# Performance work log

Hardware: AMD Instinct MI355X
Metric: run time of the kernel (lower is better)

The kernel has to match this reference:

```python
import jax, jax.numpy as jnp
import numpy as np

# module hyperparameters (from init_kwargs)
STRIDE, PAD, DIL = 1, 1, 1
GROUPS, DG = 1, 1
KH, KW = 3, 3
CIN, COUT = 256, 256


def _mdcn_forward(x, offset, mask, weight, bias):
    B, C, H, W = x.shape
    Cout = weight.shape[0]
    K = KH * KW
    Ho = (H + 2 * PAD - (DIL * (KH - 1) + 1)) // STRIDE + 1
    Wo = (W + 2 * PAD - (DIL * (KW - 1) + 1)) // STRIDE + 1
    Cg = C // DG

    # offset channel layout: ((g*K + k)*2 + {0: dy, 1: dx})
    off = offset.reshape(B, DG, KH, KW, 2, Ho, Wo)
    base_y = (jnp.arange(Ho) * STRIDE - PAD)[None, :] + DIL * jnp.arange(KH)[:, None]  # [KH,Ho]
    base_x = (jnp.arange(Wo) * STRIDE - PAD)[None, :] + DIL * jnp.arange(KW)[:, None]  # [KW,Wo]
    sy = base_y[None, None, :, None, :, None].astype(x.dtype) + off[:, :, :, :, 0]  # [B,DG,KH,KW,Ho,Wo]
    sx = base_x[None, None, None, :, None, :].astype(x.dtype) + off[:, :, :, :, 1]

    y0f = jnp.floor(sy); x0f = jnp.floor(sx)
    wy = sy - y0f; wx = sx - x0f
    y0 = y0f.astype(jnp.int32); x0 = x0f.astype(jnp.int32)

    xg = x.reshape(B, DG, Cg, H * W)

    def corner(yc, xc, w):
        valid = (yc >= 0) & (yc < H) & (xc >= 0) & (xc < W)
        idx = jnp.clip(yc, 0, H - 1) * W + jnp.clip(xc, 0, W - 1)  # [B,DG,KH,KW,Ho,Wo]
        v = jnp.take_along_axis(xg, idx.reshape(B, DG, 1, -1), axis=3)  # [B,DG,Cg,K*Ho*Wo]
        v = v.reshape(B, DG, Cg, KH, KW, Ho, Wo)
        return v * (w * valid.astype(x.dtype))[:, :, None]

    val = (corner(y0, x0, (1 - wy) * (1 - wx))
           + corner(y0, x0 + 1, (1 - wy) * wx)
           + corner(y0 + 1, x0, wy * (1 - wx))
           + corner(y0 + 1, x0 + 1, wy * wx))  # [B,DG,Cg,KH,KW,Ho,Wo]

    cols = val * mask.reshape(B, DG, 1, KH, KW, Ho, Wo)
    cols = cols.reshape(B, GROUPS, (C // GROUPS) * K, Ho * Wo)
    wg = weight.reshape(GROUPS, Cout // GROUPS, (C // GROUPS) * K)
    out = jnp.einsum('gok,bgkp->bgop', wg, cols).reshape(B, Cout, Ho, Wo)
    return out + bias[None, :, None, None]


def setup_inputs() -> dict:
    key = jax.random.key(0)
    k1, k2, k3, k4 = jax.random.split(key, 4)
    B, H, W = 4, 64, 64
    x = jax.random.normal(k1, (B, CIN, H, W), dtype=jnp.float32)
    offset = jax.random.normal(k2, (B, 2 * DG * KH * KW, H, W), dtype=jnp.float32)
    mask = jax.random.uniform(k3, (B, DG * KH * KW, H, W), dtype=jnp.float32)
    stdv = 1.0 / np.sqrt(CIN * KH * KW)
    weight = jax.random.uniform(k4, (COUT, CIN // GROUPS, KH, KW), dtype=jnp.float32,
                                minval=-stdv, maxval=stdv)
    bias = jnp.zeros((COUT,), dtype=jnp.float32)
    return {"x": x, "offset": offset, "mask": mask, "weight": weight, "bias": bias}


def reference(x, offset, mask, weight, bias):
    return _mdcn_forward(x, offset, mask, weight, bias)
```

## Files before the change

### kernel.cpp

```cpp
#include <hip/hip_runtime.h>
#include <hip/hip_bf16.h>
#include <stdint.h>

#define KDIM 2304

typedef __bf16 bf16_t;
typedef bf16_t bf16x8 __attribute__((ext_vector_type(8)));
typedef float f32x4 __attribute__((ext_vector_type(4)));
typedef float f32x2 __attribute__((ext_vector_type(2)));

__device__ __forceinline__ float b2f_lo(uint32_t u) {
  union { uint32_t i; float f; } c; c.i = u << 16; return c.f;
}
__device__ __forceinline__ float b2f_hi(uint32_t u) {
  union { uint32_t i; float f; } c; c.i = u & 0xffff0000u; return c.f;
}
__device__ __forceinline__ uint32_t pk_bf16(float a, float b) {
  __hip_bfloat162 h = __float22bfloat162_rn(make_float2(a, b));
  union { __hip_bfloat162 h; uint32_t u; } c; c.h = h; return c.u;
}

__global__ __launch_bounds__(256) void k_prep(const float* __restrict__ x,
                                              uint16_t* __restrict__ xt,
                                              const float* __restrict__ w,
                                              uint16_t* __restrict__ wt2) {
  int tid = threadIdx.x;
  if (blockIdx.x < 2048) {
    __shared__ float tile[32][65];
    int b = blockIdx.x >> 9;
    int cgrp = (blockIdx.x >> 6) & 7;
    int sgrp = blockIdx.x & 63;
    int c0 = cgrp << 5, s0 = sgrp << 6;
#pragma unroll
    for (int it = 0; it < 2; ++it) {
      int f = tid + it * 256;
      int rr = f >> 4, col = (f & 15) << 2;
      float4 v = *(const float4*)&x[((size_t)(b * 256 + c0 + rr)) * 4096 + s0 + col];
      tile[rr][col + 0] = v.x;
      tile[rr][col + 1] = v.y;
      tile[rr][col + 2] = v.z;
      tile[rr][col + 3] = v.w;
    }
    __syncthreads();
    int sp = tid >> 2, cg = tid & 3;
    uint4 o;
    o.x = pk_bf16(tile[cg * 8 + 0][sp], tile[cg * 8 + 1][sp]);
    o.y = pk_bf16(tile[cg * 8 + 2][sp], tile[cg * 8 + 3][sp]);
    o.z = pk_bf16(tile[cg * 8 + 4][sp], tile[cg * 8 + 5][sp]);
    o.w = pk_bf16(tile[cg * 8 + 6][sp], tile[cg * 8 + 7][sp]);
    *(uint4*)&xt[((size_t)b * 4096 + s0 + sp) * 256 + c0 + cg * 8] = o;
  } else {
    int i = blockIdx.x - 2048;
    int tap = i >> 2, w64 = i & 3;
    uint16_t* dst = wt2 + (size_t)i * 16384;
#pragma unroll
    for (int s = 0; s < 8; ++s) {
      int slot = tid + s * 256;
      int lane = slot & 63;
      int kh = (slot >> 6) & 1, strip = slot >> 7;
      int row = strip * 16 + (lane & 15);
      int cin0 = w64 * 64 + kh * 32 + ((lane >> 4) << 3);
      const float* src = w + (size_t)row * KDIM + (size_t)cin0 * 9 + tap;
      uint4 o;
      o.x = pk_bf16(src[0 * 9], src[1 * 9]);
      o.y = pk_bf16(src[2 * 9], src[3 * 9]);
      o.z = pk_bf16(src[4 * 9], src[5 * 9]);
      o.w = pk_bf16(src[6 * 9], src[7 * 9]);
      *(uint4*)(dst + (size_t)slot * 8) = o;
    }
  }
}

__device__ __forceinline__ void mk_corners(int tap, int p, int ho,
                                           const float* s_off, const float* s_msk,
                                           float cw[4], int cpo[4]) {
  int kh = tap / 3, kw = tap - kh * 3;
  float dy = s_off[(2 * tap) * 64 + p];
  float dx = s_off[(2 * tap + 1) * 64 + p];
  float mm = s_msk[tap * 64 + p];
  float sy = (float)(ho - 1 + kh) + dy;
  float sx = (float)(p - 1 + kw) + dx;
  float fy = floorf(sy), fx = floorf(sx);
  int y0 = (int)fy, x0 = (int)fx;
  float wy = sy - fy, wx = sx - fx;
#pragma unroll
  for (int cy = 0; cy < 2; ++cy) {
#pragma unroll
    for (int cx = 0; cx < 2; ++cx) {
      int y = y0 + cy, xx = x0 + cx;
      float wgt = (cy ? wy : 1.f - wy) * (cx ? wx : 1.f - wx) * mm;
      bool v = ((unsigned)y < 64u) && ((unsigned)xx < 64u);
      wgt = v ? wgt : 0.f;
      int yc = min(max(y, 0), 63), xc = min(max(xx, 0), 63);
      cw[cy * 2 + cx] = wgt;
      cpo[cy * 2 + cx] = ((yc << 6) + xc) * 256;
    }
  }
}

__global__ __launch_bounds__(1024, 4) void k_fused(const uint16_t* __restrict__ xt,
                                                   const uint16_t* __restrict__ wt2,
                                                   const float* __restrict__ off,
                                                   const float* __restrict__ msk,
                                                   const float* __restrict__ bias,
                                                   float* __restrict__ out) {
  __shared__ __align__(16) uint16_t Bs[2][64][64];
  __shared__ float s_off[18 * 64];
  __shared__ float s_msk[9 * 64];

  int tid = threadIdx.x;
  int swz = ((int)blockIdx.x & 7) * 32 + ((int)blockIdx.x >> 3);
  int b = swz >> 6, ho = swz & 63;

  const float* offb = off + (size_t)b * 18 * 4096 + ho * 64;
  for (int i = tid; i < 18 * 64; i += 1024)
    s_off[i] = offb[(size_t)(i >> 6) * 4096 + (i & 63)];
  const float* mskb = msk + (size_t)b * 9 * 4096 + ho * 64;
  for (int i = tid; i < 9 * 64; i += 1024)
    s_msk[i] = mskb[(size_t)(i >> 6) * 4096 + (i & 63)];

  int lane = tid & 63, strip = tid >> 6;
  int q = lane >> 4, r = lane & 15;
  int p = tid >> 4, cg = tid & 15;
  const uint16_t* xtb = xt + (size_t)b * 4096 * 256 + cg * 4;
  int bcol = (((cg >> 1) ^ (p & 7)) << 3) + ((cg & 1) << 2);

  f32x4 acc[4];
#pragma unroll
  for (int ni = 0; ni < 4; ++ni) acc[ni] = f32x4{0.f, 0.f, 0.f, 0.f};

  __syncthreads();

  float cw[4];
  int cpo[4];
  uint2 dnv[4];
  bf16x8 AFA[2], AFB[2];

  int c0 = (q ^ (r & 7)) << 3;
  int c1 = c0 ^ 32;

  mk_corners(0, p, ho, s_off, s_msk, cw, cpo);
#pragma unroll
  for (int c = 0; c < 4; ++c) dnv[c] = *(const uint2*)(xtb + cpo[c]);
  {
    const uint16_t* wp = wt2 + strip * 1024 + lane * 8;
    AFA[0] = *(const bf16x8*)(wp);
    AFA[1] = *(const bf16x8*)(wp + 512);
  }
  {
    f32x2 a0 = {0.f, 0.f}, a1 = {0.f, 0.f};
#pragma unroll
    for (int c = 0; c < 4; ++c) {
      f32x2 wc = {cw[c], cw[c]};
      a0 += wc * f32x2{b2f_lo(dnv[c].x), b2f_hi(dnv[c].x)};
      a1 += wc * f32x2{b2f_lo(dnv[c].y), b2f_hi(dnv[c].y)};
    }
    uint2 o;
    o.x = pk_bf16(a0.x, a0.y);
    o.y = pk_bf16(a1.x, a1.y);
    *(uint2*)&Bs[0][p][bcol] = o;
  }
  __syncthreads();

#define BODY(IEXPR, AFC, AFN)                                                   \
  {                                                                             \
    const int i_ = (IEXPR);                                                     \
    if (i_ < 35) {                                                              \
      int nx = i_ + 1;                                                          \
      if ((nx & 3) == 0) mk_corners(nx >> 2, p, ho, s_off, s_msk, cw, cpo);     \
      int chw = (nx & 3) << 6;                                                  \
      _Pragma("unroll")                                                         \
      for (int c = 0; c < 4; ++c) dnv[c] = *(const uint2*)(xtb + cpo[c] + chw); \
      const uint16_t* wp = wt2 + (size_t)nx * 16384 + strip * 1024 + lane * 8;  \
      AFN[0] = *(const bf16x8*)(wp);                                            \
      AFN[1] = *(const bf16x8*)(wp + 512);                                      \
    }                                                                           \
    {                                                                           \
      const uint16_t* bsrow = &Bs[(IEXPR) & 1][0][0];                           \
      _Pragma("unroll")                                                         \
      for (int ni = 0; ni < 4; ++ni) {                                          \
        bf16x8 b0 = *(const bf16x8*)(bsrow + (ni * 16 + r) * 64 + c0);          \
        bf16x8 b1 = *(const bf16x8*)(bsrow + (ni * 16 + r) * 64 + c1);          \
        acc[ni] = __builtin_amdgcn_mfma_f32_16x16x32_bf16(AFC[0], b0, acc[ni], 0, 0, 0); \
        acc[ni] = __builtin_amdgcn_mfma_f32_16x16x32_bf16(AFC[1], b1, acc[ni], 0, 0, 0); \
      }                                                                         \
    }                                                                           \
    if (i_ < 35) {                                                              \
      f32x2 a0 = {0.f, 0.f}, a1 = {0.f, 0.f};                                   \
      _Pragma("unroll")                                                         \
      for (int c = 0; c < 4; ++c) {                                             \
        f32x2 wc = {cw[c], cw[c]};                                              \
        a0 += wc * f32x2{b2f_lo(dnv[c].x), b2f_hi(dnv[c].x)};                   \
        a1 += wc * f32x2{b2f_lo(dnv[c].y), b2f_hi(dnv[c].y)};                   \
      }                                                                         \
      uint2 o;                                                                  \
      o.x = pk_bf16(a0.x, a0.y);                                                \
      o.y = pk_bf16(a1.x, a1.y);                                                \
      *(uint2*)&Bs[1 - ((IEXPR) & 1)][p][bcol] = o;                             \
    }                                                                           \
    __syncthreads();                                                            \
  }

#pragma unroll 1
  for (int ii = 0; ii < 18; ++ii) {
    BODY(2 * ii, AFA, AFB);
    BODY(2 * ii + 1, AFB, AFA);
  }
#undef BODY

#pragma unroll
  for (int j = 0; j < 4; ++j) {
    int m = strip * 16 + q * 4 + j;
    float bv = bias[m];
#pragma unroll
    for (int ni = 0; ni < 4; ++ni) {
      out[((size_t)(b * 256 + m)) * 4096 + ho * 64 + ni * 16 + r] = acc[ni][j] + bv;
    }
  }
}

extern "C" void kernel_launch(void* const* d_in, const int* in_sizes, int n_in,
                              void* d_out, int out_size, void* d_ws, size_t ws_size,
                              hipStream_t stream) {
  (void)in_sizes; (void)n_in; (void)out_size; (void)ws_size;
  const float* x      = (const float*)d_in[0];
  const float* offset = (const float*)d_in[1];
  const float* mask   = (const float*)d_in[2];
  const float* weight = (const float*)d_in[3];
  const float* bias   = (const float*)d_in[4];
  float* out = (float*)d_out;

  uint8_t* ws = (uint8_t*)d_ws;
  uint16_t* xt  = (uint16_t*)ws;
  uint16_t* wt2 = (uint16_t*)(ws + 8388608);

  k_prep<<<dim3(2084), 256, 0, stream>>>(x, xt, weight, wt2);
  k_fused<<<dim3(256), 1024, 0, stream>>>(xt, wt2, offset, mask, bias, out);
}
```

Measured before the change: 133.4 us.

## Deepen gather prefetch to two stages and coalesce weight repack via LDS

The fused kernel's main loop now prefetches the bilinear corner gathers two iterations ahead, using double-buffered corner weights and offsets, and is unrolled over tap groups with statically resolved buffers. It also issues all B-fragment LDS reads before the MFMAs and raises wave priority around them. The weight-prep blocks now use one block per output row, staging the row in shared memory so global reads are coalesced instead of strided. This costs more registers, which may reduce occupancy, and makes the loop schedule more complex.

```diff
diff --git a/kernel.cpp b/kernel.cpp
--- a/kernel.cpp
+++ b/kernel.cpp
@@ -50,23 +50,25 @@
     o.w = pk_bf16(tile[cg * 8 + 6][sp], tile[cg * 8 + 7][sp]);
     *(uint4*)&xt[((size_t)b * 4096 + s0 + sp) * 256 + c0 + cg * 8] = o;
   } else {
-    int i = blockIdx.x - 2048;
-    int tap = i >> 2, w64 = i & 3;
-    uint16_t* dst = wt2 + (size_t)i * 16384;
-#pragma unroll
-    for (int s = 0; s < 8; ++s) {
-      int slot = tid + s * 256;
-      int lane = slot & 63;
-      int kh = (slot >> 6) & 1, strip = slot >> 7;
-      int row = strip * 16 + (lane & 15);
-      int cin0 = w64 * 64 + kh * 32 + ((lane >> 4) << 3);
-      const float* src = w + (size_t)row * KDIM + (size_t)cin0 * 9 + tap;
+    __shared__ float wl[2304];
+    int row = blockIdx.x - 2048;
+    const float* wrow = w + (size_t)row * KDIM;
+    for (int i2 = tid; i2 < 2304; i2 += 256) wl[i2] = wrow[i2];
+    __syncthreads();
+    int strip = row >> 4, r16 = row & 15;
+    for (int c = tid; c < 288; c += 256) {
+      int tap = c >> 5, rem = c & 31;
+      int w64 = rem >> 3, kh = (rem >> 2) & 1, seg = rem & 3;
+      int i = tap * 4 + w64;
+      int cin0 = w64 * 64 + kh * 32 + seg * 8;
+      int lanex = seg * 16 + r16;
+      uint16_t* dst = wt2 + (size_t)i * 16384 + (size_t)(strip * 128 + kh * 64 + lanex) * 8;
       uint4 o;
-      o.x = pk_bf16(src[0 * 9], src[1 * 9]);
-      o.y = pk_bf16(src[2 * 9], src[3 * 9]);
-      o.z = pk_bf16(src[4 * 9], src[5 * 9]);
-      o.w = pk_bf16(src[6 * 9], src[7 * 9]);
-      *(uint4*)(dst + (size_t)slot * 8) = o;
+      o.x = pk_bf16(wl[(cin0 + 0) * 9 + tap], wl[(cin0 + 1) * 9 + tap]);
+      o.y = pk_bf16(wl[(cin0 + 2) * 9 + tap], wl[(cin0 + 3) * 9 + tap]);
+      o.z = pk_bf16(wl[(cin0 + 4) * 9 + tap], wl[(cin0 + 5) * 9 + tap]);
+      o.w = pk_bf16(wl[(cin0 + 6) * 9 + tap], wl[(cin0 + 7) * 9 + tap]);
+      *(uint4*)dst = o;
     }
   }
 }
@@ -131,29 +133,31 @@
 
   __syncthreads();
 
-  float cw[4];
-  int cpo[4];
-  uint2 dnv[4];
-  bf16x8 AFA[2], AFB[2];
+  float cwA[4], cwB[4];
+  int cpoA[4], cpoB[4];
+  uint2 dnvE[4], dnvO[4];
+  bf16x8 AFE[2], AFO[2];
 
   int c0 = (q ^ (r & 7)) << 3;
   int c1 = c0 ^ 32;
 
-  mk_corners(0, p, ho, s_off, s_msk, cw, cpo);
-#pragma unroll
-  for (int c = 0; c < 4; ++c) dnv[c] = *(const uint2*)(xtb + cpo[c]);
+  mk_corners(0, p, ho, s_off, s_msk, cwA, cpoA);
+#pragma unroll
+  for (int c = 0; c < 4; ++c) dnvE[c] = *(const uint2*)(xtb + cpoA[c]);
+#pragma unroll
+  for (int c = 0; c < 4; ++c) dnvO[c] = *(const uint2*)(xtb + cpoA[c] + 64);
   {
     const uint16_t* wp = wt2 + strip * 1024 + lane * 8;
-    AFA[0] = *(const bf16x8*)(wp);
-    AFA[1] = *(const bf16x8*)(wp + 512);
+    AFE[0] = *(const bf16x8*)(wp);
+    AFE[1] = *(const bf16x8*)(wp + 512);
   }
   {
     f32x2 a0 = {0.f, 0.f}, a1 = {0.f, 0.f};
 #pragma unroll
     for (int c = 0; c < 4; ++c) {
-      f32x2 wc = {cw[c], cw[c]};
-      a0 += wc * f32x2{b2f_lo(dnv[c].x), b2f_hi(dnv[c].x)};
-      a1 += wc * f32x2{b2f_lo(dnv[c].y), b2f_hi(dnv[c].y)};
+      f32x2 wc = {cwA[c], cwA[c]};
+      a0 += wc * f32x2{b2f_lo(dnvE[c].x), b2f_hi(dnvE[c].x)};
+      a1 += wc * f32x2{b2f_lo(dnvE[c].y), b2f_hi(dnvE[c].y)};
     }
     uint2 o;
     o.x = pk_bf16(a0.x, a0.y);
@@ -162,50 +166,74 @@
   }
   __syncthreads();
 
-#define BODY(IEXPR, AFC, AFN)                                                   \
+#define BODY(I, AFC, AFN, DNB, DNI, CWB, CWI, CPOI, DOMK, DODNV, DOAF, DOBL)    \
   {                                                                             \
-    const int i_ = (IEXPR);                                                     \
-    if (i_ < 35) {                                                              \
-      int nx = i_ + 1;                                                          \
-      if ((nx & 3) == 0) mk_corners(nx >> 2, p, ho, s_off, s_msk, cw, cpo);     \
-      int chw = (nx & 3) << 6;                                                  \
-      _Pragma("unroll")                                                         \
-      for (int c = 0; c < 4; ++c) dnv[c] = *(const uint2*)(xtb + cpo[c] + chw); \
-      const uint16_t* wp = wt2 + (size_t)nx * 16384 + strip * 1024 + lane * 8;  \
+    if (DOMK) mk_corners(((I) + 2) >> 2, p, ho, s_off, s_msk, CWI, CPOI);       \
+    if (DODNV) {                                                                \
+      const int chw = (((I) + 2) & 3) << 6;                                     \
+      DNI[0] = *(const uint2*)(xtb + CPOI[0] + chw);                            \
+      DNI[1] = *(const uint2*)(xtb + CPOI[1] + chw);                            \
+      DNI[2] = *(const uint2*)(xtb + CPOI[2] + chw);                            \
+      DNI[3] = *(const uint2*)(xtb + CPOI[3] + chw);                            \
+    }                                                                           \
+    if (DOAF) {                                                                 \
+      const uint16_t* wp = wt2 + (size_t)((I) + 1) * 16384 + strip * 1024 + lane * 8; \
       AFN[0] = *(const bf16x8*)(wp);                                            \
       AFN[1] = *(const bf16x8*)(wp + 512);                                      \
     }                                                                           \
     {                                                                           \
-      const uint16_t* bsrow = &Bs[(IEXPR) & 1][0][0];                           \
-      _Pragma("unroll")                                                         \
-      for (int ni = 0; ni < 4; ++ni) {                                          \
-        bf16x8 b0 = *(const bf16x8*)(bsrow + (ni * 16 + r) * 64 + c0);          \
-        bf16x8 b1 = *(const bf16x8*)(bsrow + (ni * 16 + r) * 64 + c1);          \
-        acc[ni] = __builtin_amdgcn_mfma_f32_16x16x32_bf16(AFC[0], b0, acc[ni], 0, 0, 0); \
-        acc[ni] = __builtin_amdgcn_mfma_f32_16x16x32_bf16(AFC[1], b1, acc[ni], 0, 0, 0); \
-      }                                                                         \
-    }                                                                           \
-    if (i_ < 35) {                                                              \
+      const uint16_t* bsrow = &Bs[(I) & 1][0][0];                               \
+      bf16x8 b00 = *(const bf16x8*)(bsrow + (r) * 64 + c0);                     \
+      bf16x8 b01 = *(const bf16x8*)(bsrow + (r) * 64 + c1);                     \
+      bf16x8 b10 = *(const bf16x8*)(bsrow + (16 + r) * 64 + c0);                \
+      bf16x8 b11 = *(const bf16x8*)(bsrow + (16 + r) * 64 + c1);                \
+      bf16x8 b20 = *(const bf16x8*)(bsrow + (32 + r) * 64 + c0);                \
+      bf16x8 b21 = *(const bf16x8*)(bsrow + (32 + r) * 64 + c1);                \
+      bf16x8 b30 = *(const bf16x8*)(bsrow + (48 + r) * 64 + c0);                \
+      bf16x8 b31 = *(const bf16x8*)(bsrow + (48 + r) * 64 + c1);                \
+      __builtin_amdgcn_s_setprio(1);                                            \
+      acc[0] = __builtin_amdgcn_mfma_f32_16x16x32_bf16(AFC[0], b00, acc[0], 0, 0, 0); \
+      acc[1] = __builtin_amdgcn_mfma_f32_16x16x32_bf16(AFC[0], b10, acc[1], 0, 0, 0); \
+      acc[2] = __builtin_amdgcn_mfma_f32_16x16x32_bf16(AFC[0], b20, acc[2], 0, 0, 0); \
+      acc[3] = __builtin_amdgcn_mfma_f32_16x16x32_bf16(AFC[0], b30, acc[3], 0, 0, 0); \
+      acc[0] = __builtin_amdgcn_mfma_f32_16x16x32_bf16(AFC[1], b01, acc[0], 0, 0, 0); \
+      acc[1] = __builtin_amdgcn_mfma_f32_16x16x32_bf16(AFC[1], b11, acc[1], 0, 0, 0); \
+      acc[2] = __builtin_amdgcn_mfma_f32_16x16x32_bf16(AFC[1], b21, acc[2], 0, 0, 0); \
+      acc[3] = __builtin_amdgcn_mfma_f32_16x16x32_bf16(AFC[1], b31, acc[3], 0, 0, 0); \
+      __builtin_amdgcn_s_setprio(0);                                            \
+    }                                                                           \
+    if (DOBL) {                                                                 \
       f32x2 a0 = {0.f, 0.f}, a1 = {0.f, 0.f};                                   \
       _Pragma("unroll")                                                         \
       for (int c = 0; c < 4; ++c) {                                             \
-        f32x2 wc = {cw[c], cw[c]};                                              \
-        a0 += wc * f32x2{b2f_lo(dnv[c].x), b2f_hi(dnv[c].x)};                   \
-        a1 += wc * f32x2{b2f_lo(dnv[c].y), b2f_hi(dnv[c].y)};                   \
+        f32x2 wc = {CWB[c], CWB[c]};                                            \
+        a0 += wc * f32x2{b2f_lo(DNB[c].x), b2f_hi(DNB[c].x)};                   \
+        a1 += wc * f32x2{b2f_lo(DNB[c].y), b2f_hi(DNB[c].y)};                   \
       }                                                                         \
       uint2 o;                                                                  \
       o.x = pk_bf16(a0.x, a0.y);                                                \
       o.y = pk_bf16(a1.x, a1.y);                                                \
-      *(uint2*)&Bs[1 - ((IEXPR) & 1)][p][bcol] = o;                             \
+      *(uint2*)&Bs[((I) + 1) & 1][p][bcol] = o;                                 \
     }                                                                           \
     __syncthreads();                                                            \
   }
 
 #pragma unroll 1
-  for (int ii = 0; ii < 18; ++ii) {
-    BODY(2 * ii, AFA, AFB);
-    BODY(2 * ii + 1, AFB, AFA);
-  }
+  for (int ii = 0; ii < 4; ++ii) {
+    int i0 = 8 * ii;
+    BODY(i0 + 0, AFE, AFO, dnvO, dnvE, cwA, cwA, cpoA, 0, 1, 1, 1)
+    BODY(i0 + 1, AFO, AFE, dnvE, dnvO, cwA, cwA, cpoA, 0, 1, 1, 1)
+    BODY(i0 + 2, AFE, AFO, dnvO, dnvE, cwA, cwB, cpoB, 1, 1, 1, 1)
+    BODY(i0 + 3, AFO, AFE, dnvE, dnvO, cwB, cwB, cpoB, 0, 1, 1, 1)
+    BODY(i0 + 4, AFE, AFO, dnvO, dnvE, cwB, cwB, cpoB, 0, 1, 1, 1)
+    BODY(i0 + 5, AFO, AFE, dnvE, dnvO, cwB, cwB, cpoB, 0, 1, 1, 1)
+    BODY(i0 + 6, AFE, AFO, dnvO, dnvE, cwB, cwA, cpoA, 1, 1, 1, 1)
+    BODY(i0 + 7, AFO, AFE, dnvE, dnvO, cwA, cwA, cpoA, 0, 1, 1, 1)
+  }
+  BODY(32, AFE, AFO, dnvO, dnvE, cwA, cwA, cpoA, 0, 1, 1, 1)
+  BODY(33, AFO, AFE, dnvE, dnvO, cwA, cwA, cpoA, 0, 1, 1, 1)
+  BODY(34, AFE, AFO, dnvO, dnvE, cwA, cwA, cpoA, 0, 0, 1, 1)
+  BODY(35, AFO, AFE, dnvE, dnvO, cwA, cwA, cpoA, 0, 0, 0, 0)
 #undef BODY
 
 #pragma unroll
@@ -234,6 +262,6 @@
   uint16_t* xt  = (uint16_t*)ws;
   uint16_t* wt2 = (uint16_t*)(ws + 8388608);
 
-  k_prep<<<dim3(2084), 256, 0, stream>>>(x, xt, weight, wt2);
+  k_prep<<<dim3(2304), 256, 0, stream>>>(x, xt, weight, wt2);
   k_fused<<<dim3(256), 1024, 0, stream>>>(xt, wt2, offset, mask, bias, out);
 }
```

Result: slower. 167.1 us (+25.2%).
